# Kernel tuning notes

Measured on AMD Instinct MI355X. Metric: run time of the kernel, lower is better.

## Reference

```python
import jax, jax.numpy as jnp
import numpy as np

N = 100000   # nodes
E = 800000   # directed edges (before self-loops)
D = 64       # hidden_dim
NUM_ROUNDS = 4
EPS = 1e-5


def setup_inputs() -> dict:
    key = jax.random.key(0)
    k0, k1, k2 = jax.random.split(key, 3)
    x = jax.random.normal(k0, (N, D), dtype=jnp.float32)
    edge_index = jax.random.randint(k1, (2, E), 0, N, dtype=jnp.int32)
    W = jax.random.normal(k2, (D, D), dtype=jnp.float32) * (1.0 / np.sqrt(D))
    b = jnp.zeros((D,), dtype=jnp.float32)
    gamma = jnp.ones((D,), dtype=jnp.float32)
    beta = jnp.zeros((D,), dtype=jnp.float32)
    return {"x": x, "edge_index": edge_index, "W": W, "b": b,
            "gamma": gamma, "beta": beta, "num_rounds": NUM_ROUNDS}


def reference(x, edge_index, W, b, gamma, beta, num_rounds):
    n = x.shape[0]
    # GCNConv: add self-loops, symmetric degree normalization D^-1/2 (A+I) D^-1/2
    loops = jnp.arange(n, dtype=edge_index.dtype)
    src = jnp.concatenate([edge_index[0], loops])  # [E+N] message sources
    dst = jnp.concatenate([edge_index[1], loops])  # [E+N] message targets
    deg = jax.ops.segment_sum(jnp.ones_like(dst, dtype=x.dtype), dst, num_segments=n)
    dis = jnp.where(deg > 0, jax.lax.rsqrt(deg), 0.0)  # deg^-1/2, 0 for isolated
    norm = dis[src] * dis[dst]                          # [E+N] edge weights

    for _ in range(num_rounds):
        h = x @ W                                                      # [N, D]
        msgs = h[src] * norm[:, None]                                  # gather [E+N, D]
        agg = jax.ops.segment_sum(msgs, dst, num_segments=n) + b      # scatter-add
        # LayerNorm over feature dim
        mu = agg.mean(axis=-1, keepdims=True)
        var = agg.var(axis=-1, keepdims=True)
        x = (agg - mu) * jax.lax.rsqrt(var + EPS) * gamma + beta
    return x
```

## Files before the change

### kernel.cpp

```cpp
#include <hip/hip_runtime.h>

#define D 64
#define EPSV 1e-5f
#define SLOTP 16
#define SLOTS2 24
#define BSH 9
#define BNODES (1 << BSH)
#define BCAP 8192
#define SRCBITS 17

typedef _Float16 f16;
typedef _Float16 f16x8 __attribute__((ext_vector_type(8)));
typedef float f32x4 __attribute__((ext_vector_type(4)));


__global__ void k_init(int* gcnt, int nbk) {
    int i = blockIdx.x * blockDim.x + threadIdx.x;
    if (i < nbk) gcnt[i] = 0;
}

__global__ __launch_bounds__(256) void k_binA(
    const int* __restrict__ src, const int* __restrict__ dst,
    int* __restrict__ gcnt, unsigned* __restrict__ breg, int e, int nbk) {
    __shared__ int bcnt[256];
    __shared__ int gbase[256];
    const int tid = threadIdx.x;
    if (tid < nbk) bcnt[tid] = 0;
    __syncthreads();

    const int per = (e + gridDim.x - 1) / gridDim.x;
    const int lo = blockIdx.x * per;
    const int hi = min(e, lo + per);

    for (int i = lo + tid; i < hi; i += 256)
        atomicAdd(&bcnt[dst[i] >> BSH], 1);
    __syncthreads();

    if (tid < nbk) {
        int c = bcnt[tid];
        gbase[tid] = (c > 0) ? atomicAdd(&gcnt[tid], c) : 0;
        bcnt[tid] = 0;
    }
    __syncthreads();

    for (int i = lo + tid; i < hi; i += 256) {
        int d_ = dst[i], s_ = src[i];
        int bkt = d_ >> BSH;
        int p = gbase[bkt] + atomicAdd(&bcnt[bkt], 1);
        if (p < BCAP)
            breg[(size_t)bkt * BCAP + p] =
                ((unsigned)(d_ & (BNODES - 1)) << SRCBITS) | (unsigned)s_;
    }
}

__global__ __launch_bounds__(256) void k_binB(
    const int* __restrict__ gcnt, const unsigned* __restrict__ breg,
    unsigned* __restrict__ slots, unsigned* __restrict__ slots2,
    int* __restrict__ cursor, int n) {
    __shared__ int scnt[BNODES];
    __shared__ unsigned sbuf[BNODES][SLOTP];
    const int tid = threadIdx.x;
    const int bkt = blockIdx.x;
    const int base = bkt << BSH;
    const int nloc = min(BNODES, n - base);

    for (int i = tid; i < BNODES; i += 256) scnt[i] = 0;
    __syncthreads();

    const int cnt = min(gcnt[bkt], BCAP);
    const unsigned* reg = breg + (size_t)bkt * BCAP;
    for (int i = tid; i < cnt; i += 256) {
        unsigned v = reg[i];
        int ld = v >> SRCBITS;
        unsigned s = v & ((1u << SRCBITS) - 1);
        int p = atomicAdd(&scnt[ld], 1);
        if (p < SLOTP) sbuf[ld][p] = s;
        else if (p < SLOTP + SLOTS2)
            slots2[(size_t)(base + ld) * SLOTS2 + (p - SLOTP)] = s;
    }
    __syncthreads();

    for (int i = tid; i < nloc * 4; i += 256) {
        int ld = i >> 2, part = i & 3;
        ((uint4*)(slots + (size_t)(base + ld) * SLOTP))[part] =
            ((const uint4*)sbuf[ld])[part];
    }
    for (int i = tid; i < nloc; i += 256) cursor[base + i] = scnt[i];
}

__global__ void k_dis(const int* __restrict__ cursor, float* __restrict__ disv, int n) {
    int i = blockIdx.x * blockDim.x + threadIdx.x;
    if (i < n) disv[i] = rsqrtf((float)(cursor[i] + 1));
}

__global__ void k_wpack(const float* __restrict__ W, f16* __restrict__ Wp) {
    int idx = blockIdx.x * blockDim.x + threadIdx.x;
    if (idx >= 512) return;
    int s = idx >> 8, rem = idx & 255, t = rem >> 6, l = rem & 63;
    int q = l >> 4, c = l & 15;
#pragma unroll
    for (int j = 0; j < 8; ++j) {
        int k = 32 * s + 8 * q + j;
        Wp[(size_t)idx * 8 + j] = (f16)W[k * D + 16 * t + c];
    }
}

__global__ __launch_bounds__(256) void k_xform(
    const float* __restrict__ x, const f16* __restrict__ Wp,
    const float* __restrict__ disv, f16* __restrict__ h, int n, int ntiles) {
    const int wv = blockIdx.x * 4 + (threadIdx.x >> 6);
    const int lane = threadIdx.x & 63;
    const int q = lane >> 4, c = lane & 15;

    const f16x8* wp = (const f16x8*)Wp;
    f16x8 w0 = wp[0 * 64 + lane], w1 = wp[1 * 64 + lane];
    f16x8 w2 = wp[2 * 64 + lane], w3 = wp[3 * 64 + lane];
    f16x8 w4 = wp[4 * 64 + lane], w5 = wp[5 * 64 + lane];
    f16x8 w6 = wp[6 * 64 + lane], w7 = wp[7 * 64 + lane];

#pragma unroll
    for (int tt = 0; tt < 2; ++tt) {
        const int tile = wv * 2 + tt;
        if (tile >= ntiles) break;
        const int row0 = tile * 16;
        const int rA = (row0 + c < n) ? (row0 + c) : (n - 1);

        const float4* xr = (const float4*)(x + (size_t)rA * D);
        float4 u0 = xr[2 * q], u1 = xr[2 * q + 1];
        float4 u2 = xr[8 + 2 * q], u3 = xr[9 + 2 * q];
        f16x8 a0 = (f16x8){(f16)u0.x, (f16)u0.y, (f16)u0.z, (f16)u0.w,
                           (f16)u1.x, (f16)u1.y, (f16)u1.z, (f16)u1.w};
        f16x8 a1 = (f16x8){(f16)u2.x, (f16)u2.y, (f16)u2.z, (f16)u2.w,
                           (f16)u3.x, (f16)u3.y, (f16)u3.z, (f16)u3.w};

        f32x4 d0 = {0,0,0,0}, d1 = {0,0,0,0}, d2 = {0,0,0,0}, d3 = {0,0,0,0};
        d0 = __builtin_amdgcn_mfma_f32_16x16x32_f16(a0, w0, d0, 0, 0, 0);
        d1 = __builtin_amdgcn_mfma_f32_16x16x32_f16(a0, w1, d1, 0, 0, 0);
        d2 = __builtin_amdgcn_mfma_f32_16x16x32_f16(a0, w2, d2, 0, 0, 0);
        d3 = __builtin_amdgcn_mfma_f32_16x16x32_f16(a0, w3, d3, 0, 0, 0);
        d0 = __builtin_amdgcn_mfma_f32_16x16x32_f16(a1, w4, d0, 0, 0, 0);
        d1 = __builtin_amdgcn_mfma_f32_16x16x32_f16(a1, w5, d1, 0, 0, 0);
        d2 = __builtin_amdgcn_mfma_f32_16x16x32_f16(a1, w6, d2, 0, 0, 0);
        d3 = __builtin_amdgcn_mfma_f32_16x16x32_f16(a1, w7, d3, 0, 0, 0);

        f32x4 dvv = *(const f32x4*)(disv + row0 + 4 * q);
#pragma unroll
        for (int r = 0; r < 4; ++r) {
            int row = row0 + q * 4 + r;
            if (row < n) {
                f16* hr = h + (size_t)row * D + c;
                hr[0]  = (f16)(d0[r] * dvv[r]);
                hr[16] = (f16)(d1[r] * dvv[r]);
                hr[32] = (f16)(d2[r] * dvv[r]);
                hr[48] = (f16)(d3[r] * dvv[r]);
            }
        }
    }
}

template<bool LAST>
__global__ __launch_bounds__(256) void k_fuse(
    const f16* __restrict__ h, const unsigned* __restrict__ slots,
    const unsigned* __restrict__ slots2, const int* __restrict__ cursor,
    const float* __restrict__ disv,
    const float* __restrict__ bb, const float* __restrict__ gamma,
    const float* __restrict__ beta, const f16* __restrict__ Wp,
    float* __restrict__ out, f16* __restrict__ hnext, int n) {
    __shared__ __align__(16) f16 ylds[32][72];

    const int tid = threadIdx.x;
    const int grp = tid >> 3;
    const int fl  = tid & 7;
    const int w = blockIdx.x * 32 + grp;
    const bool act = (w < n);

    if (act) {
        const int jb = w * SLOTP;
        const int dg = cursor[w];
        const int dgp = (dg < SLOTP) ? dg : SLOTP;

        float acc[8];
        {
            f16x8 sv = *(const f16x8*)(h + (size_t)w * D + fl * 8);
#pragma unroll
            for (int f = 0; f < 8; ++f) acc[f] = (float)sv[f];
        }

        uint4 s0 = *(const uint4*)(slots + jb);
        uint4 s1 = *(const uint4*)(slots + jb + 4);
        uint4 s2 = *(const uint4*)(slots + jb + 8);
        const unsigned idx[12] = {s0.x, s0.y, s0.z, s0.w,
                                  s1.x, s1.y, s1.z, s1.w,
                                  s2.x, s2.y, s2.z, s2.w};
        f16x8 v[12];
#pragma unroll
        for (int k = 0; k < 12; ++k) {
            unsigned u = (k < dg) ? idx[k] : 0u;
            v[k] = *(const f16x8*)(h + (size_t)u * D + fl * 8);
        }
#pragma unroll
        for (int k = 0; k < 12; ++k) {
            float m = (k < dg) ? 1.0f : 0.0f;
#pragma unroll
            for (int f = 0; f < 8; ++f) acc[f] += m * (float)v[k][f];
        }
        if (dgp > 12) {
            uint4 sr = *(const uint4*)(slots + jb + 12);
            const unsigned uu[4] = {sr.x, sr.y, sr.z, sr.w};
#pragma unroll
            for (int k = 0; k < 4; ++k) {
                unsigned u = (12 + k < dgp) ? uu[k] : 0u;
                float m = (12 + k < dgp) ? 1.0f : 0.0f;
                f16x8 vv = *(const f16x8*)(h + (size_t)u * D + fl * 8);
#pragma unroll
                for (int f = 0; f < 8; ++f) acc[f] += m * (float)vv[f];
            }
        }
        if (dg > SLOTP) {
            const unsigned* r2 = slots2 + (size_t)w * SLOTS2;
            int dg2 = dg - SLOTP; if (dg2 > SLOTS2) dg2 = SLOTS2;
#pragma unroll
            for (int base = 0; base < SLOTS2; base += 4) {
                if (base < dg2) {
                    uint4 sr = *(const uint4*)(r2 + base);
                    const unsigned uu[4] = {sr.x, sr.y, sr.z, sr.w};
#pragma unroll
                    for (int k = 0; k < 4; ++k) {
                        unsigned u = (base + k < dg2) ? uu[k] : 0u;
                        float m = (base + k < dg2) ? 1.0f : 0.0f;
                        f16x8 vv = *(const f16x8*)(h + (size_t)u * D + fl * 8);
#pragma unroll
                        for (int f = 0; f < 8; ++f) acc[f] += m * (float)vv[f];
                    }
                }
            }
        }

        const float dv = disv[w];
        const float4 b0 = ((const float4*)bb)[fl * 2],    b1 = ((const float4*)bb)[fl * 2 + 1];
        const float4 g0 = ((const float4*)gamma)[fl * 2], g1 = ((const float4*)gamma)[fl * 2 + 1];
        const float4 e0 = ((const float4*)beta)[fl * 2],  e1 = ((const float4*)beta)[fl * 2 + 1];
        const float bs[8] = {b0.x, b0.y, b0.z, b0.w, b1.x, b1.y, b1.z, b1.w};
        const float gs[8] = {g0.x, g0.y, g0.z, g0.w, g1.x, g1.y, g1.z, g1.w};
        const float es[8] = {e0.x, e0.y, e0.z, e0.w, e1.x, e1.y, e1.z, e1.w};

#pragma unroll
        for (int f = 0; f < 8; ++f) acc[f] = acc[f] * dv + bs[f];

        float s = 0.0f;
#pragma unroll
        for (int f = 0; f < 8; ++f) s += acc[f];
#pragma unroll
        for (int m = 1; m < 8; m <<= 1) s += __shfl_xor(s, m);
        float mu = s * (1.0f / 64.0f);
        float dd[8], qv = 0.0f;
#pragma unroll
        for (int f = 0; f < 8; ++f) { dd[f] = acc[f] - mu; qv += dd[f] * dd[f]; }
#pragma unroll
        for (int m = 1; m < 8; m <<= 1) qv += __shfl_xor(qv, m);
        float rstd = rsqrtf(qv * (1.0f / 64.0f) + EPSV);

        if (LAST) {
            float4 o0, o1;
            o0.x = dd[0] * rstd * gs[0] + es[0]; o0.y = dd[1] * rstd * gs[1] + es[1];
            o0.z = dd[2] * rstd * gs[2] + es[2]; o0.w = dd[3] * rstd * gs[3] + es[3];
            o1.x = dd[4] * rstd * gs[4] + es[4]; o1.y = dd[5] * rstd * gs[5] + es[5];
            o1.z = dd[6] * rstd * gs[6] + es[6]; o1.w = dd[7] * rstd * gs[7] + es[7];
            float4* orow = (float4*)(out + (size_t)w * D);
            orow[fl * 2] = o0; orow[fl * 2 + 1] = o1;
        } else {
            f16x8 yv;
#pragma unroll
            for (int f = 0; f < 8; ++f) yv[f] = (f16)(dd[f] * rstd * gs[f] + es[f]);
            *(f16x8*)(&ylds[grp][fl * 8]) = yv;
        }
    }
    if (LAST) return;

    __syncthreads();

    const int wv = tid >> 6;
    const int lane = tid & 63;
    const int q = lane >> 4, c = lane & 15;

    const f16x8* wp = (const f16x8*)Wp;
    f16x8 wlo = wp[wv * 64 + lane];
    f16x8 whi = wp[(4 + wv) * 64 + lane];

    const int row0 = blockIdx.x * 32;
#pragma unroll
    for (int rt = 0; rt < 2; ++rt) {
        f16x8 a0 = *(const f16x8*)(&ylds[rt * 16 + c][q * 8]);
        f16x8 a1 = *(const f16x8*)(&ylds[rt * 16 + c][32 + q * 8]);
        f32x4 d = {0, 0, 0, 0};
        d = __builtin_amdgcn_mfma_f32_16x16x32_f16(a0, wlo, d, 0, 0, 0);
        d = __builtin_amdgcn_mfma_f32_16x16x32_f16(a1, whi, d, 0, 0, 0);

        const int rbase = row0 + rt * 16;
        f32x4 dvv = *(const f32x4*)(disv + rbase + 4 * q);
#pragma unroll
        for (int r = 0; r < 4; ++r) {
            int row = rbase + q * 4 + r;
            if (row < n)
                hnext[(size_t)row * D + wv * 16 + c] = (f16)(d[r] * dvv[r]);
        }
    }
}


extern "C" void kernel_launch(void* const* d_in, const int* in_sizes, int n_in,
                              void* d_out, int out_size, void* d_ws, size_t ws_size,
                              hipStream_t stream) {
    const float* x0    = (const float*)d_in[0];
    const int*   ei    = (const int*)d_in[1];
    const float* W     = (const float*)d_in[2];
    const float* b     = (const float*)d_in[3];
    const float* gamma = (const float*)d_in[4];
    const float* beta  = (const float*)d_in[5];

    const int N = in_sizes[0] / D;
    const int E = in_sizes[1] / 2;
    const int* src = ei;
    const int* dst = ei + E;
    const int nbk = (N + BNODES - 1) >> BSH;

    char* ws = (char*)d_ws;
    size_t off = 0;
    auto alloc = [&](size_t bytes) {
        off = (off + 255) & ~(size_t)255;
        void* p = ws + off;
        off += bytes;
        return p;
    };
    int*      cursor = (int*)alloc((size_t)N * 4);
    unsigned* slots  = (unsigned*)alloc((size_t)N * SLOTP * 4);
    unsigned* slots2 = (unsigned*)alloc((size_t)N * SLOTS2 * 4);
    int*      gcnt   = (int*)alloc((size_t)nbk * 4);
    unsigned* breg   = (unsigned*)alloc((size_t)nbk * BCAP * 4);
    float*    disv   = (float*)alloc((size_t)(N + 32) * 4);
    f16*      Wp     = (f16*)alloc(512 * 8 * 2);
    f16*      hA     = (f16*)alloc((size_t)N * D * 2);
    f16*      hB     = (f16*)alloc((size_t)N * D * 2);
    (void)ws_size;

    const int nbN = (N + 255) / 256;

    k_init<<<1, 256, 0, stream>>>(gcnt, nbk);
    k_binA<<<128, 256, 0, stream>>>(src, dst, gcnt, breg, E, nbk);
    k_binB<<<nbk, 256, 0, stream>>>(gcnt, breg, slots, slots2, cursor, N);
    k_dis <<<nbN, 256, 0, stream>>>(cursor, disv, N);
    k_wpack<<<2, 256, 0, stream>>>(W, Wp);

    float* out = (float*)d_out;
    const int ntiles = (N + 15) / 16;
    const int nwav   = (ntiles + 1) / 2;
    const int GX = (nwav + 3) / 4;
    const int GG = (N + 31) / 32;

    k_xform<<<GX, 256, 0, stream>>>(x0, Wp, disv, hA, N, ntiles);
    k_fuse<false><<<GG, 256, 0, stream>>>(hA, slots, slots2, cursor, disv, b, gamma,
                                          beta, Wp, nullptr, hB, N);
    k_fuse<false><<<GG, 256, 0, stream>>>(hB, slots, slots2, cursor, disv, b, gamma,
                                          beta, Wp, nullptr, hA, N);
    k_fuse<false><<<GG, 256, 0, stream>>>(hA, slots, slots2, cursor, disv, b, gamma,
                                          beta, Wp, nullptr, hB, N);
    k_fuse<true><<<GG, 256, 0, stream>>>(hB, slots, slots2, cursor, disv, b, gamma,
                                         beta, Wp, out, nullptr, N);
}
```

Baseline: 219.8 us.

## Fold small prep kernels into neighbors and remap fuse blocks per XCD

Merges the W packing into the init kernel and the degree rsqrt into the binning kernel, which removes two launches. k_xform now gives each wave one tile instead of two, so it runs twice as many blocks. k_fuse remaps blockIdx so that each of the 8 XCDs handles a contiguous range of node blocks, aiming for better L2 locality on the mostly local gathers. The remap adds a little index arithmetic, and the one-tile xform loses the amortised weight loads.

After: 215.2 us. 1.02x faster.

```diff
diff --git a/kernel.cpp b/kernel.cpp
--- a/kernel.cpp
+++ b/kernel.cpp
@@ -14,9 +14,19 @@
 typedef float f32x4 __attribute__((ext_vector_type(4)));
 
 
-__global__ void k_init(int* gcnt, int nbk) {
-    int i = blockIdx.x * blockDim.x + threadIdx.x;
-    if (i < nbk) gcnt[i] = 0;
+__global__ void k_init(int* gcnt, int nbk, const float* __restrict__ W,
+                       f16* __restrict__ Wp) {
+    const int t = threadIdx.x;
+    if (t < nbk) gcnt[t] = 0;
+    for (int idx = t; idx < 512; idx += 256) {
+        int s = idx >> 8, rem = idx & 255, tt = rem >> 6, l = rem & 63;
+        int q = l >> 4, c = l & 15;
+#pragma unroll
+        for (int j = 0; j < 8; ++j) {
+            int k = 32 * s + 8 * q + j;
+            Wp[(size_t)idx * 8 + j] = (f16)W[k * D + 16 * tt + c];
+        }
+    }
 }
 
 __global__ __launch_bounds__(256) void k_binA(
@@ -56,7 +66,7 @@
 __global__ __launch_bounds__(256) void k_binB(
     const int* __restrict__ gcnt, const unsigned* __restrict__ breg,
     unsigned* __restrict__ slots, unsigned* __restrict__ slots2,
-    int* __restrict__ cursor, int n) {
+    int* __restrict__ cursor, float* __restrict__ disv, int n) {
     __shared__ int scnt[BNODES];
     __shared__ unsigned sbuf[BNODES][SLOTP];
     const int tid = threadIdx.x;
@@ -85,30 +95,18 @@
         ((uint4*)(slots + (size_t)(base + ld) * SLOTP))[part] =
             ((const uint4*)sbuf[ld])[part];
     }
-    for (int i = tid; i < nloc; i += 256) cursor[base + i] = scnt[i];
-}
-
-__global__ void k_dis(const int* __restrict__ cursor, float* __restrict__ disv, int n) {
-    int i = blockIdx.x * blockDim.x + threadIdx.x;
-    if (i < n) disv[i] = rsqrtf((float)(cursor[i] + 1));
-}
-
-__global__ void k_wpack(const float* __restrict__ W, f16* __restrict__ Wp) {
-    int idx = blockIdx.x * blockDim.x + threadIdx.x;
-    if (idx >= 512) return;
-    int s = idx >> 8, rem = idx & 255, t = rem >> 6, l = rem & 63;
-    int q = l >> 4, c = l & 15;
-#pragma unroll
-    for (int j = 0; j < 8; ++j) {
-        int k = 32 * s + 8 * q + j;
-        Wp[(size_t)idx * 8 + j] = (f16)W[k * D + 16 * t + c];
+    for (int i = tid; i < nloc; i += 256) {
+        int c = scnt[i];
+        cursor[base + i] = c;
+        disv[base + i] = rsqrtf((float)(c + 1));
     }
 }
 
 __global__ __launch_bounds__(256) void k_xform(
     const float* __restrict__ x, const f16* __restrict__ Wp,
     const float* __restrict__ disv, f16* __restrict__ h, int n, int ntiles) {
-    const int wv = blockIdx.x * 4 + (threadIdx.x >> 6);
+    const int tile = blockIdx.x * 4 + (threadIdx.x >> 6);
+    if (tile >= ntiles) return;
     const int lane = threadIdx.x & 63;
     const int q = lane >> 4, c = lane & 15;
 
@@ -118,42 +116,37 @@
     f16x8 w4 = wp[4 * 64 + lane], w5 = wp[5 * 64 + lane];
     f16x8 w6 = wp[6 * 64 + lane], w7 = wp[7 * 64 + lane];
 
-#pragma unroll
-    for (int tt = 0; tt < 2; ++tt) {
-        const int tile = wv * 2 + tt;
-        if (tile >= ntiles) break;
-        const int row0 = tile * 16;
-        const int rA = (row0 + c < n) ? (row0 + c) : (n - 1);
-
-        const float4* xr = (const float4*)(x + (size_t)rA * D);
-        float4 u0 = xr[2 * q], u1 = xr[2 * q + 1];
-        float4 u2 = xr[8 + 2 * q], u3 = xr[9 + 2 * q];
-        f16x8 a0 = (f16x8){(f16)u0.x, (f16)u0.y, (f16)u0.z, (f16)u0.w,
-                           (f16)u1.x, (f16)u1.y, (f16)u1.z, (f16)u1.w};
-        f16x8 a1 = (f16x8){(f16)u2.x, (f16)u2.y, (f16)u2.z, (f16)u2.w,
-                           (f16)u3.x, (f16)u3.y, (f16)u3.z, (f16)u3.w};
-
-        f32x4 d0 = {0,0,0,0}, d1 = {0,0,0,0}, d2 = {0,0,0,0}, d3 = {0,0,0,0};
-        d0 = __builtin_amdgcn_mfma_f32_16x16x32_f16(a0, w0, d0, 0, 0, 0);
-        d1 = __builtin_amdgcn_mfma_f32_16x16x32_f16(a0, w1, d1, 0, 0, 0);
-        d2 = __builtin_amdgcn_mfma_f32_16x16x32_f16(a0, w2, d2, 0, 0, 0);
-        d3 = __builtin_amdgcn_mfma_f32_16x16x32_f16(a0, w3, d3, 0, 0, 0);
-        d0 = __builtin_amdgcn_mfma_f32_16x16x32_f16(a1, w4, d0, 0, 0, 0);
-        d1 = __builtin_amdgcn_mfma_f32_16x16x32_f16(a1, w5, d1, 0, 0, 0);
-        d2 = __builtin_amdgcn_mfma_f32_16x16x32_f16(a1, w6, d2, 0, 0, 0);
-        d3 = __builtin_amdgcn_mfma_f32_16x16x32_f16(a1, w7, d3, 0, 0, 0);
-
-        f32x4 dvv = *(const f32x4*)(disv + row0 + 4 * q);
-#pragma unroll
-        for (int r = 0; r < 4; ++r) {
-            int row = row0 + q * 4 + r;
-            if (row < n) {
-                f16* hr = h + (size_t)row * D + c;
-                hr[0]  = (f16)(d0[r] * dvv[r]);
-                hr[16] = (f16)(d1[r] * dvv[r]);
-                hr[32] = (f16)(d2[r] * dvv[r]);
-                hr[48] = (f16)(d3[r] * dvv[r]);
-            }
+    const int row0 = tile * 16;
+    const int rA = (row0 + c < n) ? (row0 + c) : (n - 1);
+
+    const float4* xr = (const float4*)(x + (size_t)rA * D);
+    float4 u0 = xr[2 * q], u1 = xr[2 * q + 1];
+    float4 u2 = xr[8 + 2 * q], u3 = xr[9 + 2 * q];
+    f16x8 a0 = (f16x8){(f16)u0.x, (f16)u0.y, (f16)u0.z, (f16)u0.w,
+                       (f16)u1.x, (f16)u1.y, (f16)u1.z, (f16)u1.w};
+    f16x8 a1 = (f16x8){(f16)u2.x, (f16)u2.y, (f16)u2.z, (f16)u2.w,
+                       (f16)u3.x, (f16)u3.y, (f16)u3.z, (f16)u3.w};
+
+    f32x4 d0 = {0,0,0,0}, d1 = {0,0,0,0}, d2 = {0,0,0,0}, d3 = {0,0,0,0};
+    d0 = __builtin_amdgcn_mfma_f32_16x16x32_f16(a0, w0, d0, 0, 0, 0);
+    d1 = __builtin_amdgcn_mfma_f32_16x16x32_f16(a0, w1, d1, 0, 0, 0);
+    d2 = __builtin_amdgcn_mfma_f32_16x16x32_f16(a0, w2, d2, 0, 0, 0);
+    d3 = __builtin_amdgcn_mfma_f32_16x16x32_f16(a0, w3, d3, 0, 0, 0);
+    d0 = __builtin_amdgcn_mfma_f32_16x16x32_f16(a1, w4, d0, 0, 0, 0);
+    d1 = __builtin_amdgcn_mfma_f32_16x16x32_f16(a1, w5, d1, 0, 0, 0);
+    d2 = __builtin_amdgcn_mfma_f32_16x16x32_f16(a1, w6, d2, 0, 0, 0);
+    d3 = __builtin_amdgcn_mfma_f32_16x16x32_f16(a1, w7, d3, 0, 0, 0);
+
+    f32x4 dvv = *(const f32x4*)(disv + row0 + 4 * q);
+#pragma unroll
+    for (int r = 0; r < 4; ++r) {
+        int row = row0 + q * 4 + r;
+        if (row < n) {
+            f16* hr = h + (size_t)row * D + c;
+            hr[0]  = (f16)(d0[r] * dvv[r]);
+            hr[16] = (f16)(d1[r] * dvv[r]);
+            hr[32] = (f16)(d2[r] * dvv[r]);
+            hr[48] = (f16)(d3[r] * dvv[r]);
         }
     }
 }
@@ -165,13 +158,17 @@
     const float* __restrict__ disv,
     const float* __restrict__ bb, const float* __restrict__ gamma,
     const float* __restrict__ beta, const f16* __restrict__ Wp,
-    float* __restrict__ out, f16* __restrict__ hnext, int n) {
+    float* __restrict__ out, f16* __restrict__ hnext, int n,
+    int sq, int sr) {
     __shared__ __align__(16) f16 ylds[32][72];
+
+    const int xb = blockIdx.x & 7, kb = blockIdx.x >> 3;
+    const int bid = (xb < sr ? xb * (sq + 1) : sr * (sq + 1) + (xb - sr) * sq) + kb;
 
     const int tid = threadIdx.x;
     const int grp = tid >> 3;
     const int fl  = tid & 7;
-    const int w = blockIdx.x * 32 + grp;
+    const int w = bid * 32 + grp;
     const bool act = (w < n);
 
     if (act) {
@@ -205,8 +202,8 @@
             for (int f = 0; f < 8; ++f) acc[f] += m * (float)v[k][f];
         }
         if (dgp > 12) {
-            uint4 sr = *(const uint4*)(slots + jb + 12);
-            const unsigned uu[4] = {sr.x, sr.y, sr.z, sr.w};
+            uint4 sr4 = *(const uint4*)(slots + jb + 12);
+            const unsigned uu[4] = {sr4.x, sr4.y, sr4.z, sr4.w};
 #pragma unroll
             for (int k = 0; k < 4; ++k) {
                 unsigned u = (12 + k < dgp) ? uu[k] : 0u;
@@ -222,8 +219,8 @@
 #pragma unroll
             for (int base = 0; base < SLOTS2; base += 4) {
                 if (base < dg2) {
-                    uint4 sr = *(const uint4*)(r2 + base);
-                    const unsigned uu[4] = {sr.x, sr.y, sr.z, sr.w};
+                    uint4 sr4 = *(const uint4*)(r2 + base);
+                    const unsigned uu[4] = {sr4.x, sr4.y, sr4.z, sr4.w};
 #pragma unroll
                     for (int k = 0; k < 4; ++k) {
                         unsigned u = (base + k < dg2) ? uu[k] : 0u;
@@ -287,7 +284,7 @@
     f16x8 wlo = wp[wv * 64 + lane];
     f16x8 whi = wp[(4 + wv) * 64 + lane];
 
-    const int row0 = blockIdx.x * 32;
+    const int row0 = bid * 32;
 #pragma unroll
     for (int rt = 0; rt < 2; ++rt) {
         f16x8 a0 = *(const f16x8*)(&ylds[rt * 16 + c][q * 8]);
@@ -343,27 +340,23 @@
     f16*      hB     = (f16*)alloc((size_t)N * D * 2);
     (void)ws_size;
 
-    const int nbN = (N + 255) / 256;
-
-    k_init<<<1, 256, 0, stream>>>(gcnt, nbk);
+    k_init<<<1, 256, 0, stream>>>(gcnt, nbk, W, Wp);
     k_binA<<<128, 256, 0, stream>>>(src, dst, gcnt, breg, E, nbk);
-    k_binB<<<nbk, 256, 0, stream>>>(gcnt, breg, slots, slots2, cursor, N);
-    k_dis <<<nbN, 256, 0, stream>>>(cursor, disv, N);
-    k_wpack<<<2, 256, 0, stream>>>(W, Wp);
+    k_binB<<<nbk, 256, 0, stream>>>(gcnt, breg, slots, slots2, cursor, disv, N);
 
     float* out = (float*)d_out;
     const int ntiles = (N + 15) / 16;
-    const int nwav   = (ntiles + 1) / 2;
-    const int GX = (nwav + 3) / 4;
+    const int GX = (ntiles + 3) / 4;
     const int GG = (N + 31) / 32;
+    const int sq = GG / 8, sr = GG % 8;
 
     k_xform<<<GX, 256, 0, stream>>>(x0, Wp, disv, hA, N, ntiles);
     k_fuse<false><<<GG, 256, 0, stream>>>(hA, slots, slots2, cursor, disv, b, gamma,
-                                          beta, Wp, nullptr, hB, N);
+                                          beta, Wp, nullptr, hB, N, sq, sr);
     k_fuse<false><<<GG, 256, 0, stream>>>(hB, slots, slots2, cursor, disv, b, gamma,
-                                          beta, Wp, nullptr, hA, N);
+                                          beta, Wp, nullptr, hA, N, sq, sr);
     k_fuse<false><<<GG, 256, 0, stream>>>(hA, slots, slots2, cursor, disv, b, gamma,
-                                          beta, Wp, nullptr, hB, N);
+                                          beta, Wp, nullptr, hB, N, sq, sr);
     k_fuse<true><<<GG, 256, 0, stream>>>(hB, slots, slots2, cursor, disv, b, gamma,
-                                         beta, Wp, out, nullptr, N);
-}
+                                         beta, Wp, out, nullptr, N, sq, sr);
+}
```
